# Kernel optimization log

Hardware: AMD Instinct MI355X
Metric: run time of the kernel (lower is better)

## Reference

```python
import jax, jax.numpy as jnp
import numpy as np

T, B, N, M, OUT = 128, 512, 256, 512, 1


def _lin_params(key, out_dim, in_dim, scale=0.05):
    kw, kb = jax.random.split(key)
    W = jax.random.normal(kw, (out_dim, in_dim), dtype=jnp.float32) * scale
    b = jax.random.normal(kb, (out_dim,), dtype=jnp.float32) * scale
    return W, b


def setup_inputs() -> dict:
    key = jax.random.key(0)
    ks = jax.random.split(key, 10)
    x = jax.random.normal(ks[0], (T, B, N), dtype=jnp.float32)
    h0 = jnp.zeros((B, M), dtype=jnp.float32)
    c0 = jnp.zeros((B, M), dtype=jnp.float32)
    # nn.LSTM(n, m): weight_ih (4m,n), weight_hh (4m,m), biases (4m,), gate order i,f,g,o
    Wih, b_ih = _lin_params(ks[1], 4 * M, N)
    Whh, b_hh = _lin_params(ks[2], 4 * M, M)
    We_w, We_b = _lin_params(ks[3], T, 2 * M)   # We: Linear(2m, T)
    Ue_w, Ue_b = _lin_params(ks[4], T, T)       # Ue: Linear(T, T)
    ve_w, ve_b = _lin_params(ks[5], 1, T)       # ve: Linear(T, 1)
    Ud_w, Ud_b = _lin_params(ks[6], M, M)       # Ud: Linear(m, m)
    vd_w, vd_b = _lin_params(ks[7], 1, M)       # vd: Linear(m, 1)
    out_w, out_b = _lin_params(ks[8], OUT, M)   # out: Linear(m, output_dim)
    return dict(x=x, h0=h0, c0=c0, Wih=Wih, Whh=Whh, b_ih=b_ih, b_hh=b_hh,
                We_w=We_w, We_b=We_b, Ue_w=Ue_w, Ue_b=Ue_b, ve_w=ve_w, ve_b=ve_b,
                Ud_w=Ud_w, Ud_b=Ud_b, vd_w=vd_w, vd_b=vd_b, out_w=out_w, out_b=out_b)


def reference(x, h0, c0, Wih, Whh, b_ih, b_hh, We_w, We_b, Ue_w, Ue_b,
              ve_w, ve_b, Ud_w, Ud_b, vd_w, vd_b, out_w, out_b):
    # x: (T, B, n) time-major; dropout_p=0 (eval) -> identity.
    x_perm = jnp.transpose(x, (1, 2, 0))                      # (B, n, T)
    # Ue(x) is independent of the recurrent state; compute once (same math).
    Ue_x = jnp.einsum('bnt,st->bns', x_perm, Ue_w) + Ue_b     # (B, n, T)

    def step(carry, xt):
        h, c = carry                                          # (B, m) each
        hc = jnp.concatenate([h, c], axis=-1)                 # (B, 2m)
        we = hc @ We_w.T + We_b                               # (B, T)
        e = jnp.tanh(we[:, None, :] + Ue_x) @ ve_w[0] + ve_b[0]   # (B, n)
        alpha = jax.nn.softmax(e, axis=1)                     # softmax over n
        x_tilde = alpha * xt                                  # (B, n)
        # LSTM cell (PyTorch gate order i, f, g, o)
        gates = x_tilde @ Wih.T + b_ih + h @ Whh.T + b_hh     # (B, 4m)
        i, f, g, o = jnp.split(gates, 4, axis=-1)
        c_new = jax.nn.sigmoid(f) * c + jax.nn.sigmoid(i) * jnp.tanh(g)
        h_new = jax.nn.sigmoid(o) * jnp.tanh(c_new)
        return (h_new, c_new), h_new

    (_, _), h_seq = jax.lax.scan(step, (h0, c0), x)           # h_seq: (T, B, m)

    # temporal attention over encoder hidden states
    h = jnp.transpose(h_seq, (1, 0, 2))                       # (B, T, m)
    l = jnp.tanh(h @ Ud_w.T + Ud_b) @ vd_w[0] + vd_b[0]       # (B, T)
    beta = jax.nn.softmax(l, axis=1)                          # (B, T)
    ctx = jnp.einsum('bt,btm->bm', beta, h)                   # (B, m)
    logits = ctx @ out_w.T + out_b                            # (B, output_dim)
    return logits, beta
```

## Files before the change

kernel.cpp:

```cpp
#include <hip/hip_runtime.h>
#include <math.h>

#define T_ 128
#define B_ 512
#define N_ 256
#define M_ 512
#define G_ 2048
#define NBLK 256
#define GSZ 32
#define KC_ 24

typedef unsigned long long ull;
typedef __attribute__((ext_vector_type(8))) short short8v;
typedef __attribute__((ext_vector_type(4))) float float4v;

__device__ __forceinline__ float ld_dev(const float* p) {
    return __hip_atomic_load(const_cast<float*>(p), __ATOMIC_RELAXED,
                             __HIP_MEMORY_SCOPE_AGENT);
}
__device__ __forceinline__ void st_dev(float* p, float v) {
    __hip_atomic_store(p, v, __ATOMIC_RELAXED, __HIP_MEMORY_SCOPE_AGENT);
}
__device__ __forceinline__ ull ld_dev64(const ull* p) {
    return __hip_atomic_load(const_cast<ull*>(p), __ATOMIC_RELAXED,
                             __HIP_MEMORY_SCOPE_AGENT);
}
__device__ __forceinline__ void st_dev64(ull* p, ull v) {
    __hip_atomic_store(p, v, __ATOMIC_RELAXED, __HIP_MEMORY_SCOPE_AGENT);
}

__device__ __forceinline__ float fast_tanh(float x) {
    float e = __expf(2.f * x);
    return 1.f - __fdividef(2.f, e + 1.f);
}
__device__ __forceinline__ float fast_sig(float x) {
    return __fdividef(1.f, 1.f + __expf(-x));
}

__device__ __forceinline__ unsigned short bf16_rne(float f) {
    unsigned u = __float_as_uint(f);
    return (unsigned short)((u + 0x7FFFu + ((u >> 16) & 1u)) >> 16);
}
__device__ __forceinline__ float bf16_tof(unsigned short h) {
    return __uint_as_float(((unsigned)h) << 16);
}
__device__ __forceinline__ ull pack4(const unsigned short* s) {
    return (ull)s[0] | ((ull)s[1] << 16) | ((ull)s[2] << 32) | ((ull)s[3] << 48);
}

__device__ __forceinline__ void group_bar(int* gbar, int goal) {
    __syncthreads();
    if (threadIdx.x == 0) {
        asm volatile("s_waitcnt vmcnt(0)" ::: "memory");
        __hip_atomic_fetch_add(gbar, 1, __ATOMIC_RELAXED,
                               __HIP_MEMORY_SCOPE_AGENT);
        while (__hip_atomic_load(gbar, __ATOMIC_RELAXED,
                                 __HIP_MEMORY_SCOPE_AGENT) < goal) {
            __builtin_amdgcn_s_sleep(1);
        }
    }
    __syncthreads();
}

__global__ __launch_bounds__(256) void prep_bg(
    const float* __restrict__ bih, const float* __restrict__ bhh,
    float* __restrict__ bg)
{
    int rp = blockIdx.x * 256 + threadIdx.x;
    if (rp < 2048) {
        int m = rp >> 2, g = rp & 3;
        int row = g * 512 + m;
        bg[rp] = bih[row] + bhh[row];
    }
}

__global__ __launch_bounds__(256) void prep_wt(
    const float* __restrict__ Wih, const float* __restrict__ Whh,
    uint4* __restrict__ Wt_hi, uint4* __restrict__ Wt_lo)
{
    int uid = blockIdx.x * 256 + threadIdx.x;
    int ct = uid / (KC_ * 64);
    int rem = uid % (KC_ * 64);
    int kc = rem >> 6, lane = rem & 63;
    int col = ct * 16 + (lane & 15);
    int m = col >> 2, gi = col & 3;
    int grow = gi * 512 + m;
    int quad = lane >> 4;
    union { unsigned short s[8]; uint4 v; } hi, lo;
#pragma unroll
    for (int j = 0; j < 8; j++) {
        int k = kc * 32 + quad * 8 + j;
        float v = (k < 256) ? Wih[(size_t)grow * 256 + k]
                            : Whh[(size_t)grow * 512 + (k - 256)];
        hi.s[j] = bf16_rne(v);
        lo.s[j] = bf16_rne(v - bf16_tof(hi.s[j]));
    }
    Wt_hi[uid] = hi.v;
    Wt_lo[uid] = lo.v;
}

__global__ __launch_bounds__(256) void prep_wep(
    const float* __restrict__ We_w, float* __restrict__ We_p)
{
    int idx = blockIdx.x * 256 + threadIdx.x;
    int q = idx >> 9, rest = idx & 511, s = rest >> 2, j = rest & 3;
    We_p[idx] = We_w[s * 1024 + q * 4 + j];
}

__global__ __launch_bounds__(256) void ue_pre(
    const float* __restrict__ x, const float* __restrict__ Ue_w,
    const float* __restrict__ Ue_b, unsigned* __restrict__ ue_pk)
{
    const int b = blockIdx.y;
    const int s0 = blockIdx.x * 32;
    const int n = threadIdx.x;
    __shared__ float xs[32][256];
    __shared__ float uws[32][32];

    float acc[32];
#pragma unroll
    for (int i = 0; i < 32; i++) acc[i] = 0.f;

#pragma unroll 1
    for (int tc = 0; tc < 4; tc++) {
        __syncthreads();
#pragma unroll
        for (int tt = 0; tt < 32; tt++)
            xs[tt][n] = x[(size_t)(tc * 32 + tt) * (B_ * N_) + b * N_ + n];
#pragma unroll
        for (int q = 0; q < 4; q++) {
            int e = q * 256 + n;
            int s = e >> 5, tt = e & 31;
            uws[s][tt] = Ue_w[(s0 + s) * T_ + tc * 32 + tt];
        }
        __syncthreads();
        float xr[32];
#pragma unroll
        for (int tt = 0; tt < 32; tt++) xr[tt] = xs[tt][n];
#pragma unroll
        for (int s = 0; s < 32; s++) {
            float a = acc[s];
#pragma unroll
            for (int tt = 0; tt < 32; tt++) a += xr[tt] * uws[s][tt];
            acc[s] = a;
        }
    }
#pragma unroll
    for (int i = 0; i < 16; i++) {
        float v0 = (acc[2 * i] + Ue_b[s0 + 2 * i]) * 2.0f;
        float v1 = (acc[2 * i + 1] + Ue_b[s0 + 2 * i + 1]) * 2.0f;
        unsigned pk = (unsigned)bf16_rne(v0) | ((unsigned)bf16_rne(v1) << 16);
        ue_pk[((size_t)b * 64 + (s0 >> 1) + i) * 256 + n] = pk;
    }
}

__global__ __launch_bounds__(512, 1) void scan_persist(
    const float* __restrict__ x, const float* __restrict__ h0,
    const float* __restrict__ We_p, const float* __restrict__ We_b,
    const float* __restrict__ ve_w, const unsigned* __restrict__ ue_pk,
    const short8v* __restrict__ Wt_hi, const short8v* __restrict__ Wt_lo,
    const float* __restrict__ bg,
    float* __restrict__ cbuf, float* __restrict__ hseq,
    ull* __restrict__ At_hi, ull* __restrict__ At_lo, int* bar)
{
    const int tid = threadIdx.x;
    const int blk = blockIdx.x;
    const int g = blk >> 5;
    const int sg = blk & 31;
    int* gbar = bar + g * 32;

    __shared__ __align__(16) float hcA[1024];
    __shared__ __align__(16) float hcB[1024];
    __shared__ float wepartA[512];
    __shared__ float wepartB[512];
    __shared__ __align__(16) float wv[2][256];
    __shared__ float red[16];
    __shared__ float xs[2][256];
    __shared__ float gates_s[64][65];

    const int bA = g * 64 + sg * 2;
    const int bB = bA + 1;
    const int s_ = tid & 127;
    const int qr = tid >> 7;
    const int half = tid >> 8;
    const int tt = tid & 255;
    const int lane = tid & 63;
    const int w = tid >> 6;
    const int rtC = g * 4 + (w & 3);
    const int ctA = sg * 4 + (w >> 2) * 2;
    const int ctB = ctA + 1;
    const int quad = lane >> 4;
    const int mi_c = tid & 15;
    const int b_l0 = tid >> 4;
    const int cidx0 = (g * 64 + b_l0) * M_ + sg * 16 + mi_c;
    const int cidx1 = cidx0 + 32 * M_;

    if (tid < 128) {
        float v = 2.0f * ve_w[tid];
        wv[0][tid * 2 + 1] = v;
        wv[1][tid * 2 + 1] = v;
    }

    const float bgi = bg[sg * 64 + mi_c * 4 + 0];
    const float bgf = bg[sg * 64 + mi_c * 4 + 1];
    const float bgc = bg[sg * 64 + mi_c * 4 + 2];
    const float bgo = bg[sg * 64 + mi_c * 4 + 3];

    unsigned ureg[64];
    {
        const unsigned* up = ue_pk + ((size_t)(bA + half) * 64) * 256 + tt;
#pragma unroll
        for (int i = 0; i < 64; i++) ureg[i] = up[(size_t)i * 256];
    }

#pragma unroll 1
    for (int t = 0; t < T_; t++) {
        const float* hprev = t ? (hseq + (size_t)(t - 1) * (B_ * M_)) : h0;

        {
            hcA[tid]       = ld_dev(hprev + bA * M_ + tid);
            hcA[512 + tid] = ld_dev(cbuf + bA * M_ + tid);
            hcB[tid]       = ld_dev(hprev + bB * M_ + tid);
            hcB[512 + tid] = ld_dev(cbuf + bB * M_ + tid);
            float xv = x[(size_t)t * (B_ * N_) + (bA + half) * N_ + tt];
            __syncthreads();

            if (tid < 128) {
                int rowsel = tid >> 6;
                int q2 = tid & 63;
                int kc = 8 + (q2 >> 2), qd = q2 & 3;
                const float* hcX = rowsel ? hcB : hcA;
                int mb = (kc - 8) * 32 + qd * 8;
                float v[8];
#pragma unroll
                for (int j = 0; j < 8; j++) v[j] = hcX[mb + j];
                int b2 = bA + rowsel;
                int rt = b2 >> 4;
                int ln = qd * 16 + (b2 & 15);
                size_t uidx = ((size_t)(rt * KC_ + kc) * 64 + ln) * 2;
                unsigned short hi[8], lo[8];
#pragma unroll
                for (int j = 0; j < 8; j++) {
                    hi[j] = bf16_rne(v[j]);
                    lo[j] = bf16_rne(v[j] - bf16_tof(hi[j]));
                }
                st_dev64(At_hi + uidx,     pack4(hi));
                st_dev64(At_hi + uidx + 1, pack4(hi + 4));
                st_dev64(At_lo + uidx,     pack4(lo));
                st_dev64(At_lo + uidx + 1, pack4(lo + 4));
            }

            float accA = 0.f, accB = 0.f;
            const float4* wp4 = (const float4*)We_p;
#pragma unroll 4
            for (int q = qr * 64; q < qr * 64 + 64; q++) {
                float4 wq = wp4[q * 128 + s_];
                float4 a = *(const float4*)&hcA[q * 4];
                float4 b2 = *(const float4*)&hcB[q * 4];
                accA += wq.x * a.x + wq.y * a.y + wq.z * a.z + wq.w * a.w;
                accB += wq.x * b2.x + wq.y * b2.y + wq.z * b2.z + wq.w * b2.w;
            }
            wepartA[qr * 128 + s_] = accA;
            wepartB[qr * 128 + s_] = accB;
            __syncthreads();
            if (tid < 128) {
                float wb = We_b[tid];
                wv[0][tid * 2] = (wepartA[tid] + wepartA[128 + tid]
                                + wepartA[256 + tid] + wepartA[384 + tid] + wb) * 2.0f;
                wv[1][tid * 2] = (wepartB[tid] + wepartB[128 + tid]
                                + wepartB[256 + tid] + wepartB[384 + tid] + wb) * 2.0f;
            }
            __syncthreads();

            float e = 0.f;
#pragma unroll
            for (int i = 0; i < 64; i++) {
                unsigned u = ureg[i];
                float4 q = *(const float4*)&wv[half][i * 4];
                float z0 = q.x + __uint_as_float(u << 16);
                float z1 = q.z + __uint_as_float(u & 0xFFFF0000u);
                float r0 = __builtin_amdgcn_rcpf(__expf(z0) + 1.f);
                float r1 = __builtin_amdgcn_rcpf(__expf(z1) + 1.f);
                e = fmaf(-q.y, r0, e);
                e = fmaf(-q.w, r1, e);
            }

            float m = e;
#pragma unroll
            for (int off = 32; off >= 1; off >>= 1)
                m = fmaxf(m, __shfl_xor(m, off));
            if (lane == 0) red[w] = m;
            __syncthreads();
            float mx = fmaxf(fmaxf(red[half * 4 + 0], red[half * 4 + 1]),
                             fmaxf(red[half * 4 + 2], red[half * 4 + 3]));
            float ex = __expf(e - mx);
            float sm = ex;
#pragma unroll
            for (int off = 32; off >= 1; off >>= 1)
                sm += __shfl_xor(sm, off);
            if (lane == 0) red[8 + w] = sm;
            __syncthreads();
            float denom = red[8 + half * 4 + 0] + red[8 + half * 4 + 1]
                        + red[8 + half * 4 + 2] + red[8 + half * 4 + 3];
            float alpha = __fdividef(ex, denom);
            xs[half][tt] = alpha * xv;
            __syncthreads();

            if (tid >= 128 && tid < 192) {
                int u2 = tid - 128;
                int rowsel = u2 >> 5;
                int q2 = u2 & 31;
                int kc = q2 >> 2, qd = q2 & 3;
                int nb = kc * 32 + qd * 8;
                float v[8];
#pragma unroll
                for (int j = 0; j < 8; j++) v[j] = xs[rowsel][nb + j];
                int b2 = bA + rowsel;
                int rt = b2 >> 4;
                int ln = qd * 16 + (b2 & 15);
                size_t uidx = ((size_t)(rt * KC_ + kc) * 64 + ln) * 2;
                unsigned short hi[8], lo[8];
#pragma unroll
                for (int j = 0; j < 8; j++) {
                    hi[j] = bf16_rne(v[j]);
                    lo[j] = bf16_rne(v[j] - bf16_tof(hi[j]));
                }
                st_dev64(At_hi + uidx,     pack4(hi));
                st_dev64(At_hi + uidx + 1, pack4(hi + 4));
                st_dev64(At_lo + uidx,     pack4(lo));
                st_dev64(At_lo + uidx + 1, pack4(lo + 4));
            }
        }
        group_bar(gbar, (t * 2 + 1) * GSZ);

        {
            float cold0 = ld_dev(&cbuf[cidx0]);
            float cold1 = ld_dev(&cbuf[cidx1]);

            float4v acc0 = {0.f, 0.f, 0.f, 0.f};
            float4v acc1 = {0.f, 0.f, 0.f, 0.f};

            size_t aidx = ((size_t)(rtC * KC_ + 0) * 64 + lane) * 2;
            ull pah0 = ld_dev64(At_hi + aidx), pah1 = ld_dev64(At_hi + aidx + 1);
            ull pal0 = ld_dev64(At_lo + aidx), pal1 = ld_dev64(At_lo + aidx + 1);
            short8v pw0h = Wt_hi[(ctA * KC_ + 0) * 64 + lane];
            short8v pw0l = Wt_lo[(ctA * KC_ + 0) * 64 + lane];
            short8v pw1h = Wt_hi[(ctB * KC_ + 0) * 64 + lane];
            short8v pw1l = Wt_lo[(ctB * KC_ + 0) * 64 + lane];

#pragma unroll 1
            for (int kc = 0; kc < KC_; kc++) {
                ull ah0 = pah0, ah1 = pah1, al0 = pal0, al1 = pal1;
                short8v w0h = pw0h, w0l = pw0l, w1h = pw1h, w1l = pw1l;
                if (kc + 1 < KC_) {
                    size_t ai = ((size_t)(rtC * KC_ + kc + 1) * 64 + lane) * 2;
                    pah0 = ld_dev64(At_hi + ai); pah1 = ld_dev64(At_hi + ai + 1);
                    pal0 = ld_dev64(At_lo + ai); pal1 = ld_dev64(At_lo + ai + 1);
                    pw0h = Wt_hi[(ctA * KC_ + kc + 1) * 64 + lane];
                    pw0l = Wt_lo[(ctA * KC_ + kc + 1) * 64 + lane];
                    pw1h = Wt_hi[(ctB * KC_ + kc + 1) * 64 + lane];
                    pw1l = Wt_lo[(ctB * KC_ + kc + 1) * 64 + lane];
                }
                union { ull u[2]; short8v s; } aH, aL;
                aH.u[0] = ah0; aH.u[1] = ah1;
                aL.u[0] = al0; aL.u[1] = al1;
                acc0 = __builtin_amdgcn_mfma_f32_16x16x32_bf16(aH.s, w0h, acc0, 0, 0, 0);
                acc1 = __builtin_amdgcn_mfma_f32_16x16x32_bf16(aH.s, w1h, acc1, 0, 0, 0);
                acc0 = __builtin_amdgcn_mfma_f32_16x16x32_bf16(aH.s, w0l, acc0, 0, 0, 0);
                acc1 = __builtin_amdgcn_mfma_f32_16x16x32_bf16(aH.s, w1l, acc1, 0, 0, 0);
                acc0 = __builtin_amdgcn_mfma_f32_16x16x32_bf16(aL.s, w0h, acc0, 0, 0, 0);
                acc1 = __builtin_amdgcn_mfma_f32_16x16x32_bf16(aL.s, w1h, acc1, 0, 0, 0);
            }

            const int r0 = (w & 3) * 16;
            const int c0l = (w >> 2) * 32;
#pragma unroll
            for (int r = 0; r < 4; r++) {
                gates_s[r0 + quad * 4 + r][c0l + (lane & 15)] = acc0[r];
                gates_s[r0 + quad * 4 + r][c0l + 16 + (lane & 15)] = acc1[r];
            }
            __syncthreads();

            float* hseq_t = hseq + (size_t)t * (B_ * M_);
            {
                float gi = gates_s[b_l0][mi_c * 4 + 0] + bgi;
                float gf = gates_s[b_l0][mi_c * 4 + 1] + bgf;
                float gc = gates_s[b_l0][mi_c * 4 + 2] + bgc;
                float go = gates_s[b_l0][mi_c * 4 + 3] + bgo;
                float cn = fast_sig(gf) * cold0 + fast_sig(gi) * fast_tanh(gc);
                st_dev(&cbuf[cidx0], cn);
                st_dev(&hseq_t[cidx0], fast_sig(go) * fast_tanh(cn));
            }
            {
                float gi = gates_s[b_l0 + 32][mi_c * 4 + 0] + bgi;
                float gf = gates_s[b_l0 + 32][mi_c * 4 + 1] + bgf;
                float gc = gates_s[b_l0 + 32][mi_c * 4 + 2] + bgc;
                float go = gates_s[b_l0 + 32][mi_c * 4 + 3] + bgo;
                float cn = fast_sig(gf) * cold1 + fast_sig(gi) * fast_tanh(gc);
                st_dev(&cbuf[cidx1], cn);
                st_dev(&hseq_t[cidx1], fast_sig(go) * fast_tanh(cn));
            }
        }
        group_bar(gbar, (t * 2 + 2) * GSZ);
    }
}

__global__ __launch_bounds__(256) void gemm_l(
    const float* __restrict__ A1,
    const float* __restrict__ W1,
    const float* __restrict__ bias1,
    const float* __restrict__ vw, float* __restrict__ lout)
{
    __shared__ float As[16][68];
    __shared__ float Ws[16][68];
    __shared__ float rsum[64];

    const int tid = threadIdx.x;
    const int tx = tid & 15, ty = tid >> 4;
    const int row0 = blockIdx.y * 64;
    const int col0 = blockIdx.x * 64;
    const int li = tid >> 2;
    const int lk4 = (tid & 3) * 4;

    float acc[4][4];
#pragma unroll
    for (int r = 0; r < 4; r++)
#pragma unroll
        for (int cc = 0; cc < 4; cc++) acc[r][cc] = 0.f;

    float4 av = *(const float4*)&A1[(size_t)(row0 + li) * M_ + lk4];
    float4 wvv = *(const float4*)&W1[(size_t)(col0 + li) * M_ + lk4];
#pragma unroll 1
    for (int kk = 0; kk < 512; kk += 16) {
        __syncthreads();
        As[lk4 + 0][li] = av.x; As[lk4 + 1][li] = av.y;
        As[lk4 + 2][li] = av.z; As[lk4 + 3][li] = av.w;
        Ws[lk4 + 0][li] = wvv.x; Ws[lk4 + 1][li] = wvv.y;
        Ws[lk4 + 2][li] = wvv.z; Ws[lk4 + 3][li] = wvv.w;
        __syncthreads();
        if (kk + 16 < 512) {
            av = *(const float4*)&A1[(size_t)(row0 + li) * M_ + kk + 16 + lk4];
            wvv = *(const float4*)&W1[(size_t)(col0 + li) * M_ + kk + 16 + lk4];
        }
#pragma unroll
        for (int k = 0; k < 16; k++) {
            float4 a = *(const float4*)&As[k][ty * 4];
            float4 w2 = *(const float4*)&Ws[k][tx * 4];
            acc[0][0] += a.x * w2.x; acc[0][1] += a.x * w2.y;
            acc[0][2] += a.x * w2.z; acc[0][3] += a.x * w2.w;
            acc[1][0] += a.y * w2.x; acc[1][1] += a.y * w2.y;
            acc[1][2] += a.y * w2.z; acc[1][3] += a.y * w2.w;
            acc[2][0] += a.z * w2.x; acc[2][1] += a.z * w2.y;
            acc[2][2] += a.z * w2.z; acc[2][3] += a.z * w2.w;
            acc[3][0] += a.w * w2.x; acc[3][1] += a.w * w2.y;
            acc[3][2] += a.w * w2.z; acc[3][3] += a.w * w2.w;
        }
    }

    __syncthreads();
    if (tid < 64) rsum[tid] = 0.f;
    __syncthreads();
    float part[4] = {0.f, 0.f, 0.f, 0.f};
#pragma unroll
    for (int r = 0; r < 4; r++)
#pragma unroll
        for (int cc = 0; cc < 4; cc++) {
            int gc = col0 + tx * 4 + cc;
            part[r] += fast_tanh(acc[r][cc] + bias1[gc]) * vw[gc];
        }
#pragma unroll
    for (int r = 0; r < 4; r++)
        atomicAdd(&rsum[ty * 4 + r], part[r]);
    __syncthreads();
    if (tid < 64) {
        int gr = row0 + tid;
        int b = gr & 511, t = gr >> 9;
        atomicAdd(&lout[b * 128 + t], rsum[tid]);
    }
}

__global__ __launch_bounds__(512) void final_kernel(
    const float* __restrict__ lbuf, const float* __restrict__ hseq,
    const float* __restrict__ out_w, const float* __restrict__ out_b,
    float* __restrict__ out)
{
    const int b = blockIdx.x;
    const int tid = threadIdx.x;
    __shared__ float beta_s[128];
    __shared__ float red[512];

    float lv = (tid < 128) ? lbuf[b * 128 + tid] : -1e30f;
    red[tid] = lv; __syncthreads();
    for (int off = 256; off >= 1; off >>= 1) {
        if (tid < off) red[tid] = fmaxf(red[tid], red[tid + off]);
        __syncthreads();
    }
    float mx = red[0]; __syncthreads();
    float ex = (tid < 128) ? __expf(lv - mx) : 0.f;
    red[tid] = ex; __syncthreads();
    for (int off = 256; off >= 1; off >>= 1) {
        if (tid < off) red[tid] += red[tid + off];
        __syncthreads();
    }
    float denom = red[0];
    if (tid < 128) {
        float bt = ex / denom;
        beta_s[tid] = bt;
        out[512 + b * 128 + tid] = bt;
    }
    __syncthreads();

    float ctx = 0.f;
#pragma unroll 4
    for (int t = 0; t < 128; t++)
        ctx += beta_s[t] * hseq[(size_t)t * (B_ * M_) + b * M_ + tid];

    red[tid] = ctx * out_w[tid]; __syncthreads();
    for (int off = 256; off >= 1; off >>= 1) {
        if (tid < off) red[tid] += red[tid + off];
        __syncthreads();
    }
    if (tid == 0) out[b] = red[0] + out_b[0];
}

extern "C" void kernel_launch(void* const* d_in, const int* in_sizes, int n_in,
                              void* d_out, int out_size, void* d_ws, size_t ws_size,
                              hipStream_t stream)
{
    const float* x    = (const float*)d_in[0];
    const float* h0   = (const float*)d_in[1];
    const float* c0   = (const float*)d_in[2];
    const float* Wih  = (const float*)d_in[3];
    const float* Whh  = (const float*)d_in[4];
    const float* b_ih = (const float*)d_in[5];
    const float* b_hh = (const float*)d_in[6];
    const float* We_w = (const float*)d_in[7];
    const float* We_b = (const float*)d_in[8];
    const float* Ue_w = (const float*)d_in[9];
    const float* Ue_b = (const float*)d_in[10];
    const float* ve_w = (const float*)d_in[11];
    const float* Ud_w = (const float*)d_in[13];
    const float* Ud_b = (const float*)d_in[14];
    const float* vd_w = (const float*)d_in[15];
    const float* out_w = (const float*)d_in[17];
    const float* out_b = (const float*)d_in[18];
    float* out = (float*)d_out;

    float* ws    = (float*)d_ws;
    float* ue_pk = ws;
    float* lbuf  = ws;
    float* hseq  = ue_pk + 8388608;
    float* cbuf  = hseq + 33554432;
    float* We_p  = cbuf + 262144;
    float* bgv   = We_p + 131072;
    float* At_hi = bgv + 2048;
    float* At_lo = At_hi + 196608;
    float* Wt_hi = At_lo + 196608;
    float* Wt_lo = Wt_hi + 786432;
    int*   bar   = (int*)(Wt_lo + 786432);

    hipMemcpyAsync(cbuf, c0, (size_t)B_ * M_ * 4, hipMemcpyDeviceToDevice, stream);
    hipMemsetAsync(bar, 0, 8 * 32 * 4, stream);

    prep_bg<<<8, 256, 0, stream>>>(b_ih, b_hh, bgv);
    prep_wt<<<768, 256, 0, stream>>>(Wih, Whh, (uint4*)Wt_hi, (uint4*)Wt_lo);
    prep_wep<<<512, 256, 0, stream>>>(We_w, We_p);
    ue_pre<<<dim3(4, 512), 256, 0, stream>>>(x, Ue_w, Ue_b, (unsigned*)ue_pk);

    scan_persist<<<NBLK, 512, 0, stream>>>(
        x, h0, We_p, We_b, ve_w, (const unsigned*)ue_pk,
        (const short8v*)Wt_hi, (const short8v*)Wt_lo, bgv,
        cbuf, hseq, (ull*)At_hi, (ull*)At_lo, bar);

    hipMemsetAsync(lbuf, 0, (size_t)B_ * T_ * 4, stream);
    gemm_l<<<dim3(8, 1024), 256, 0, stream>>>(hseq, Ud_w, Ud_b, vd_w, lbuf);
    final_kernel<<<512, 512, 0, stream>>>(lbuf, hseq, out_w, out_b, out);
}
```

Before: 4.520 ms.

## Compute We partials in LSTM tail with MFMA and double-buffer recurrent operands

Moves the per-step We·[h,c] projection out of the attention phase. Each block now computes partial products for its own 16-column slice of h and c with split-bf16 MFMA at the end of the previous step and writes them to a global slab; the next step sums 32 partials. The cell state now stays in registers, the h operand is packed into a double-buffered At array inside the tail, and a grid-wide start barrier is added. This drops the per-step global reload of full h/c rows and the scalar fp32 We loop, at the cost of extra global partial stores and loads plus a bigger shared-memory footprint.

Result: slower. 6.313 ms (+39.7%).

```diff
diff --git a/kernel.cpp b/kernel.cpp
--- a/kernel.cpp
+++ b/kernel.cpp
@@ -99,12 +99,27 @@
     Wt_lo[uid] = lo.v;
 }
 
-__global__ __launch_bounds__(256) void prep_wep(
-    const float* __restrict__ We_w, float* __restrict__ We_p)
-{
-    int idx = blockIdx.x * 256 + threadIdx.x;
-    int q = idx >> 9, rest = idx & 511, s = rest >> 2, j = rest & 3;
-    We_p[idx] = We_w[s * 1024 + q * 4 + j];
+__global__ __launch_bounds__(256) void prep_wes(
+    const float* __restrict__ We_w, uint4* __restrict__ Wes_hi,
+    uint4* __restrict__ Wes_lo)
+{
+    int uid = blockIdx.x * 256 + threadIdx.x;
+    int sg = uid >> 9;
+    int rem = uid & 511;
+    int st = rem >> 6, lane = rem & 63;
+    int s = st * 16 + (lane & 15);
+    int quad = lane >> 4;
+    union { unsigned short s[8]; uint4 v; } hi, lo;
+#pragma unroll
+    for (int j = 0; j < 8; j++) {
+        int kk = quad * 8 + j;
+        int k = (kk < 16) ? (sg * 16 + kk) : (512 + sg * 16 + (kk - 16));
+        float v = We_w[s * 1024 + k];
+        hi.s[j] = bf16_rne(v);
+        lo.s[j] = bf16_rne(v - bf16_tof(hi.s[j]));
+    }
+    Wes_hi[uid] = hi.v;
+    Wes_lo[uid] = lo.v;
 }
 
 __global__ __launch_bounds__(256) void ue_pre(
@@ -156,12 +171,16 @@
 
 __global__ __launch_bounds__(512, 1) void scan_persist(
     const float* __restrict__ x, const float* __restrict__ h0,
-    const float* __restrict__ We_p, const float* __restrict__ We_b,
-    const float* __restrict__ ve_w, const unsigned* __restrict__ ue_pk,
+    const float* __restrict__ c0,
+    const float* __restrict__ We_b, const float* __restrict__ ve_w,
+    const unsigned* __restrict__ ue_pk,
     const short8v* __restrict__ Wt_hi, const short8v* __restrict__ Wt_lo,
+    const short8v* __restrict__ Wes_hi, const short8v* __restrict__ Wes_lo,
     const float* __restrict__ bg,
-    float* __restrict__ cbuf, float* __restrict__ hseq,
-    ull* __restrict__ At_hi, ull* __restrict__ At_lo, int* bar)
+    float* __restrict__ hseq, float* __restrict__ wepart,
+    ull* __restrict__ At_hi0, ull* __restrict__ At_lo0,
+    ull* __restrict__ At_hi1, ull* __restrict__ At_lo1,
+    int* bar, int* gcount)
 {
     const int tid = threadIdx.x;
     const int blk = blockIdx.x;
@@ -169,19 +188,16 @@
     const int sg = blk & 31;
     int* gbar = bar + g * 32;
 
-    __shared__ __align__(16) float hcA[1024];
-    __shared__ __align__(16) float hcB[1024];
-    __shared__ float wepartA[512];
-    __shared__ float wepartB[512];
     __shared__ __align__(16) float wv[2][256];
     __shared__ float red[16];
     __shared__ float xs[2][256];
     __shared__ float gates_s[64][65];
+    __shared__ __align__(16) float hn_s[64][20];
+    __shared__ __align__(16) float cn_s[64][20];
+    __shared__ short8v wes_hi_s[512];
+    __shared__ short8v wes_lo_s[512];
 
     const int bA = g * 64 + sg * 2;
-    const int bB = bA + 1;
-    const int s_ = tid & 127;
-    const int qr = tid >> 7;
     const int half = tid >> 8;
     const int tt = tid & 255;
     const int lane = tid & 63;
@@ -206,69 +222,122 @@
     const float bgc = bg[sg * 64 + mi_c * 4 + 2];
     const float bgo = bg[sg * 64 + mi_c * 4 + 3];
 
+    wes_hi_s[tid] = Wes_hi[sg * 512 + tid];
+    wes_lo_s[tid] = Wes_lo[sg * 512 + tid];
+
+    float cst0 = c0[cidx0];
+    float cst1 = c0[cidx1];
+
     unsigned ureg[64];
     {
         const unsigned* up = ue_pk + ((size_t)(bA + half) * 64) * 256 + tt;
 #pragma unroll
         for (int i = 0; i < 64; i++) ureg[i] = up[(size_t)i * 256];
     }
+    asm volatile("s_waitcnt vmcnt(0)" ::: "memory");
+    __syncthreads();
+    if (tid == 0) {
+        __hip_atomic_fetch_add(gcount, 1, __ATOMIC_RELAXED,
+                               __HIP_MEMORY_SCOPE_AGENT);
+        while (__hip_atomic_load(gcount, __ATOMIC_RELAXED,
+                                 __HIP_MEMORY_SCOPE_AGENT) < NBLK) {
+            __builtin_amdgcn_s_sleep(1);
+        }
+    }
+    __syncthreads();
+
+    auto tail = [&](ull* nAh, ull* nAl) {
+        if (tid < 128) {
+            int rt_l = tid >> 5;
+            int q    = (tid >> 4) & 1;
+            int b_lo = tid & 15;
+            int b_local = rt_l * 16 + b_lo;
+            float v[8];
+#pragma unroll
+            for (int j = 0; j < 8; j++) v[j] = hn_s[b_local][q * 8 + j];
+            int kc = 8 + (sg >> 1);
+            int ln = (2 * (sg & 1) + q) * 16 + b_lo;
+            size_t uidx = ((size_t)((g * 4 + rt_l) * KC_ + kc) * 64 + ln) * 2;
+            unsigned short hi[8], lo[8];
+#pragma unroll
+            for (int j = 0; j < 8; j++) {
+                hi[j] = bf16_rne(v[j]);
+                lo[j] = bf16_rne(v[j] - bf16_tof(hi[j]));
+            }
+            st_dev64(nAh + uidx,     pack4(hi));
+            st_dev64(nAh + uidx + 1, pack4(hi + 4));
+            st_dev64(nAl + uidx,     pack4(lo));
+            st_dev64(nAl + uidx + 1, pack4(lo + 4));
+        }
+        {
+            int bt = w & 3;
+            int sth = (w >> 2) * 4;
+            int bb = bt * 16 + (lane & 15);
+            float a[8];
+#pragma unroll
+            for (int j = 0; j < 8; j++)
+                a[j] = (quad < 2) ? hn_s[bb][(quad & 1) * 8 + j]
+                                  : cn_s[bb][(quad & 1) * 8 + j];
+            union { unsigned short s[8]; short8v v; } ah, al;
+#pragma unroll
+            for (int j = 0; j < 8; j++) {
+                ah.s[j] = bf16_rne(a[j]);
+                al.s[j] = bf16_rne(a[j] - bf16_tof(ah.s[j]));
+            }
+            float* slab = wepart + ((size_t)(g * 32 + sg) * 64) * 128;
+#pragma unroll
+            for (int i = 0; i < 4; i++) {
+                short8v bh = wes_hi_s[(sth + i) * 64 + lane];
+                short8v bl2 = wes_lo_s[(sth + i) * 64 + lane];
+                float4v wp = {0.f, 0.f, 0.f, 0.f};
+                wp = __builtin_amdgcn_mfma_f32_16x16x32_bf16(al.v, bh, wp, 0, 0, 0);
+                wp = __builtin_amdgcn_mfma_f32_16x16x32_bf16(ah.v, bl2, wp, 0, 0, 0);
+                wp = __builtin_amdgcn_mfma_f32_16x16x32_bf16(ah.v, bh, wp, 0, 0, 0);
+                int s = (sth + i) * 16 + (lane & 15);
+                float* dst = slab + (size_t)(bt * 16 + quad * 4) * 128 + s;
+                st_dev(dst + 0 * 128, wp[0]);
+                st_dev(dst + 1 * 128, wp[1]);
+                st_dev(dst + 2 * 128, wp[2]);
+                st_dev(dst + 3 * 128, wp[3]);
+            }
+        }
+    };
+
+    {
+        int mi = tid & 15;
+        int bl = tid >> 4;
+        size_t base = (size_t)(g * 64 + bl) * M_ + sg * 16 + mi;
+        hn_s[bl][mi]      = h0[base];
+        hn_s[bl + 32][mi] = h0[base + (size_t)32 * M_];
+        cn_s[bl][mi]      = c0[base];
+        cn_s[bl + 32][mi] = c0[base + (size_t)32 * M_];
+    }
+    __syncthreads();
+    tail(At_hi0, At_lo0);
+
+    int bgoal = GSZ;
+    group_bar(gbar, bgoal); bgoal += GSZ;
 
 #pragma unroll 1
     for (int t = 0; t < T_; t++) {
-        const float* hprev = t ? (hseq + (size_t)(t - 1) * (B_ * M_)) : h0;
+        const int cur = t & 1;
+        const ull* Ah_c = cur ? At_hi1 : At_hi0;
+        const ull* Al_c = cur ? At_lo1 : At_lo0;
+        ull* nAh = cur ? At_hi0 : At_hi1;
+        ull* nAl = cur ? At_lo0 : At_lo1;
 
         {
-            hcA[tid]       = ld_dev(hprev + bA * M_ + tid);
-            hcA[512 + tid] = ld_dev(cbuf + bA * M_ + tid);
-            hcB[tid]       = ld_dev(hprev + bB * M_ + tid);
-            hcB[512 + tid] = ld_dev(cbuf + bB * M_ + tid);
             float xv = x[(size_t)t * (B_ * N_) + (bA + half) * N_ + tt];
-            __syncthreads();
-
-            if (tid < 128) {
-                int rowsel = tid >> 6;
-                int q2 = tid & 63;
-                int kc = 8 + (q2 >> 2), qd = q2 & 3;
-                const float* hcX = rowsel ? hcB : hcA;
-                int mb = (kc - 8) * 32 + qd * 8;
-                float v[8];
-#pragma unroll
-                for (int j = 0; j < 8; j++) v[j] = hcX[mb + j];
-                int b2 = bA + rowsel;
-                int rt = b2 >> 4;
-                int ln = qd * 16 + (b2 & 15);
-                size_t uidx = ((size_t)(rt * KC_ + kc) * 64 + ln) * 2;
-                unsigned short hi[8], lo[8];
-#pragma unroll
-                for (int j = 0; j < 8; j++) {
-                    hi[j] = bf16_rne(v[j]);
-                    lo[j] = bf16_rne(v[j] - bf16_tof(hi[j]));
-                }
-                st_dev64(At_hi + uidx,     pack4(hi));
-                st_dev64(At_hi + uidx + 1, pack4(hi + 4));
-                st_dev64(At_lo + uidx,     pack4(lo));
-                st_dev64(At_lo + uidx + 1, pack4(lo + 4));
-            }
-
-            float accA = 0.f, accB = 0.f;
-            const float4* wp4 = (const float4*)We_p;
-#pragma unroll 4
-            for (int q = qr * 64; q < qr * 64 + 64; q++) {
-                float4 wq = wp4[q * 128 + s_];
-                float4 a = *(const float4*)&hcA[q * 4];
-                float4 b2 = *(const float4*)&hcB[q * 4];
-                accA += wq.x * a.x + wq.y * a.y + wq.z * a.z + wq.w * a.w;
-                accB += wq.x * b2.x + wq.y * b2.y + wq.z * b2.z + wq.w * b2.w;
-            }
-            wepartA[qr * 128 + s_] = accA;
-            wepartB[qr * 128 + s_] = accB;
-            __syncthreads();
-            if (tid < 128) {
-                float wb = We_b[tid];
-                wv[0][tid * 2] = (wepartA[tid] + wepartA[128 + tid]
-                                + wepartA[256 + tid] + wepartA[384 + tid] + wb) * 2.0f;
-                wv[1][tid * 2] = (wepartB[tid] + wepartB[128 + tid]
-                                + wepartB[256 + tid] + wepartB[384 + tid] + wb) * 2.0f;
+            if (tid < 256) {
+                int half2 = tid >> 7;
+                int s = tid & 127;
+                const float* wp = wepart
+                    + ((size_t)(g * 32) * 64 + (sg * 2 + half2)) * 128 + s;
+                float sum = 0.f;
+#pragma unroll
+                for (int src = 0; src < 32; src++)
+                    sum += ld_dev(wp + (size_t)src * 64 * 128);
+                wv[half2][2 * s] = 2.0f * (sum + We_b[s]);
             }
             __syncthreads();
 
@@ -325,24 +394,21 @@
                     hi[j] = bf16_rne(v[j]);
                     lo[j] = bf16_rne(v[j] - bf16_tof(hi[j]));
                 }
-                st_dev64(At_hi + uidx,     pack4(hi));
-                st_dev64(At_hi + uidx + 1, pack4(hi + 4));
-                st_dev64(At_lo + uidx,     pack4(lo));
-                st_dev64(At_lo + uidx + 1, pack4(lo + 4));
-            }
-        }
-        group_bar(gbar, (t * 2 + 1) * GSZ);
+                st_dev64((ull*)Ah_c + uidx,     pack4(hi));
+                st_dev64((ull*)Ah_c + uidx + 1, pack4(hi + 4));
+                st_dev64((ull*)Al_c + uidx,     pack4(lo));
+                st_dev64((ull*)Al_c + uidx + 1, pack4(lo + 4));
+            }
+        }
+        group_bar(gbar, bgoal); bgoal += GSZ;
 
         {
-            float cold0 = ld_dev(&cbuf[cidx0]);
-            float cold1 = ld_dev(&cbuf[cidx1]);
-
             float4v acc0 = {0.f, 0.f, 0.f, 0.f};
             float4v acc1 = {0.f, 0.f, 0.f, 0.f};
 
             size_t aidx = ((size_t)(rtC * KC_ + 0) * 64 + lane) * 2;
-            ull pah0 = ld_dev64(At_hi + aidx), pah1 = ld_dev64(At_hi + aidx + 1);
-            ull pal0 = ld_dev64(At_lo + aidx), pal1 = ld_dev64(At_lo + aidx + 1);
+            ull pah0 = ld_dev64(Ah_c + aidx), pah1 = ld_dev64(Ah_c + aidx + 1);
+            ull pal0 = ld_dev64(Al_c + aidx), pal1 = ld_dev64(Al_c + aidx + 1);
             short8v pw0h = Wt_hi[(ctA * KC_ + 0) * 64 + lane];
             short8v pw0l = Wt_lo[(ctA * KC_ + 0) * 64 + lane];
             short8v pw1h = Wt_hi[(ctB * KC_ + 0) * 64 + lane];
@@ -354,8 +420,8 @@
                 short8v w0h = pw0h, w0l = pw0l, w1h = pw1h, w1l = pw1l;
                 if (kc + 1 < KC_) {
                     size_t ai = ((size_t)(rtC * KC_ + kc + 1) * 64 + lane) * 2;
-                    pah0 = ld_dev64(At_hi + ai); pah1 = ld_dev64(At_hi + ai + 1);
-                    pal0 = ld_dev64(At_lo + ai); pal1 = ld_dev64(At_lo + ai + 1);
+                    pah0 = ld_dev64(Ah_c + ai); pah1 = ld_dev64(Ah_c + ai + 1);
+                    pal0 = ld_dev64(Al_c + ai); pal1 = ld_dev64(Al_c + ai + 1);
                     pw0h = Wt_hi[(ctA * KC_ + kc + 1) * 64 + lane];
                     pw0l = Wt_lo[(ctA * KC_ + kc + 1) * 64 + lane];
                     pw1h = Wt_hi[(ctB * KC_ + kc + 1) * 64 + lane];
@@ -387,21 +453,29 @@
                 float gf = gates_s[b_l0][mi_c * 4 + 1] + bgf;
                 float gc = gates_s[b_l0][mi_c * 4 + 2] + bgc;
                 float go = gates_s[b_l0][mi_c * 4 + 3] + bgo;
-                float cn = fast_sig(gf) * cold0 + fast_sig(gi) * fast_tanh(gc);
-                st_dev(&cbuf[cidx0], cn);
-                st_dev(&hseq_t[cidx0], fast_sig(go) * fast_tanh(cn));
+                float cn = fast_sig(gf) * cst0 + fast_sig(gi) * fast_tanh(gc);
+                cst0 = cn;
+                float hn = fast_sig(go) * fast_tanh(cn);
+                hseq_t[cidx0] = hn;
+                hn_s[b_l0][mi_c] = hn;
+                cn_s[b_l0][mi_c] = cn;
             }
             {
                 float gi = gates_s[b_l0 + 32][mi_c * 4 + 0] + bgi;
                 float gf = gates_s[b_l0 + 32][mi_c * 4 + 1] + bgf;
                 float gc = gates_s[b_l0 + 32][mi_c * 4 + 2] + bgc;
                 float go = gates_s[b_l0 + 32][mi_c * 4 + 3] + bgo;
-                float cn = fast_sig(gf) * cold1 + fast_sig(gi) * fast_tanh(gc);
-                st_dev(&cbuf[cidx1], cn);
-                st_dev(&hseq_t[cidx1], fast_sig(go) * fast_tanh(cn));
-            }
-        }
-        group_bar(gbar, (t * 2 + 2) * GSZ);
+                float cn = fast_sig(gf) * cst1 + fast_sig(gi) * fast_tanh(gc);
+                cst1 = cn;
+                float hn = fast_sig(go) * fast_tanh(cn);
+                hseq_t[cidx1] = hn;
+                hn_s[b_l0 + 32][mi_c] = hn;
+                cn_s[b_l0 + 32][mi_c] = cn;
+            }
+            __syncthreads();
+            if (t + 1 < T_) tail(nAh, nAl);
+        }
+        group_bar(gbar, bgoal); bgoal += GSZ;
     }
 }
 
@@ -546,31 +620,36 @@
     const float* out_b = (const float*)d_in[18];
     float* out = (float*)d_out;
 
-    float* ws    = (float*)d_ws;
-    float* ue_pk = ws;
-    float* lbuf  = ws;
-    float* hseq  = ue_pk + 8388608;
-    float* cbuf  = hseq + 33554432;
-    float* We_p  = cbuf + 262144;
-    float* bgv   = We_p + 131072;
-    float* At_hi = bgv + 2048;
-    float* At_lo = At_hi + 196608;
-    float* Wt_hi = At_lo + 196608;
-    float* Wt_lo = Wt_hi + 786432;
-    int*   bar   = (int*)(Wt_lo + 786432);
-
-    hipMemcpyAsync(cbuf, c0, (size_t)B_ * M_ * 4, hipMemcpyDeviceToDevice, stream);
-    hipMemsetAsync(bar, 0, 8 * 32 * 4, stream);
+    float* ws     = (float*)d_ws;
+    float* ue_pk  = ws;
+    float* lbuf   = ws;
+    float* wepart = ws + 4194304;
+    float* hseq   = ws + 8388608;
+    float* At_hi0 = hseq + 33554432;
+    float* At_lo0 = At_hi0 + 196608;
+    float* At_hi1 = At_lo0 + 196608;
+    float* At_lo1 = At_hi1 + 196608;
+    float* Wes_hi = At_lo1 + 196608;
+    float* Wes_lo = Wes_hi + 65536;
+    float* bgv    = Wes_lo + 65536;
+    float* Wt_hi  = bgv + 2048;
+    float* Wt_lo  = Wt_hi + 786432;
+    int*   bar    = (int*)(Wt_lo + 786432);
+
+    hipMemsetAsync(bar, 0, (8 * 32 + 1) * 4, stream);
 
     prep_bg<<<8, 256, 0, stream>>>(b_ih, b_hh, bgv);
     prep_wt<<<768, 256, 0, stream>>>(Wih, Whh, (uint4*)Wt_hi, (uint4*)Wt_lo);
-    prep_wep<<<512, 256, 0, stream>>>(We_w, We_p);
+    prep_wes<<<64, 256, 0, stream>>>(We_w, (uint4*)Wes_hi, (uint4*)Wes_lo);
     ue_pre<<<dim3(4, 512), 256, 0, stream>>>(x, Ue_w, Ue_b, (unsigned*)ue_pk);
 
     scan_persist<<<NBLK, 512, 0, stream>>>(
-        x, h0, We_p, We_b, ve_w, (const unsigned*)ue_pk,
-        (const short8v*)Wt_hi, (const short8v*)Wt_lo, bgv,
-        cbuf, hseq, (ull*)At_hi, (ull*)At_lo, bar);
+        x, h0, c0, We_b, ve_w, (const unsigned*)ue_pk,
+        (const short8v*)Wt_hi, (const short8v*)Wt_lo,
+        (const short8v*)Wes_hi, (const short8v*)Wes_lo, bgv,
+        hseq, wepart,
+        (ull*)At_hi0, (ull*)At_lo0, (ull*)At_hi1, (ull*)At_lo1,
+        bar, bar + 256);
 
     hipMemsetAsync(lbuf, 0, (size_t)B_ * T_ * 4, stream);
     gemm_l<<<dim3(8, 1024), 256, 0, stream>>>(hseq, Ud_w, Ud_b, vd_w, lbuf);
```

## Overlap recurrent h@Whh MFMA with attention phase using double-buffered packed h

Applied to the files above, without the earlier changes.

Splits the LSTM gate GEMM into an x-part and an h-part. The h@Whh MFMA accumulation (16 k-chunks) now runs inside the We projection loop in phase 1, overlapping it with the attention work, and only the 8 x_tilde chunks remain after the group barrier. Each block packs its new h slice into bf16 hi/lo operand buffers at the end of the step, using ping-pong buffers so the next step can read them without an extra barrier. This shortens the critical path between the two barriers, at the cost of more register pressure and an extra shared buffer plus an initial barrier.

After: 6.327 ms. 1.4x slower.

```diff
diff --git a/kernel.cpp b/kernel.cpp
--- a/kernel.cpp
+++ b/kernel.cpp
@@ -161,7 +161,10 @@
     const short8v* __restrict__ Wt_hi, const short8v* __restrict__ Wt_lo,
     const float* __restrict__ bg,
     float* __restrict__ cbuf, float* __restrict__ hseq,
-    ull* __restrict__ At_hi, ull* __restrict__ At_lo, int* bar)
+    ull* __restrict__ Atx_hi, ull* __restrict__ Atx_lo,
+    ull* __restrict__ Ath_hi0, ull* __restrict__ Ath_lo0,
+    ull* __restrict__ Ath_hi1, ull* __restrict__ Ath_lo1,
+    int* bar)
 {
     const int tid = threadIdx.x;
     const int blk = blockIdx.x;
@@ -177,6 +180,7 @@
     __shared__ float red[16];
     __shared__ float xs[2][256];
     __shared__ float gates_s[64][65];
+    __shared__ float hn_s[64][17];
 
     const int bA = g * 64 + sg * 2;
     const int bB = bA + 1;
@@ -213,52 +217,97 @@
         for (int i = 0; i < 64; i++) ureg[i] = up[(size_t)i * 256];
     }
 
+    if (tid < 128) {
+        int rt_l = tid >> 5;
+        int q = (tid >> 4) & 1;
+        int b_lo = tid & 15;
+        int b_local = rt_l * 16 + b_lo;
+        float v[8];
+#pragma unroll
+        for (int j = 0; j < 8; j++)
+            v[j] = h0[(size_t)(g * 64 + b_local) * M_ + sg * 16 + q * 8 + j];
+        unsigned short hi[8], lo[8];
+#pragma unroll
+        for (int j = 0; j < 8; j++) {
+            hi[j] = bf16_rne(v[j]);
+            lo[j] = bf16_rne(v[j] - bf16_tof(hi[j]));
+        }
+        int kh = sg >> 1;
+        int ln = (2 * (sg & 1) + q) * 16 + b_lo;
+        size_t uidx = ((size_t)((g * 4 + rt_l) * 16 + kh) * 64 + ln) * 2;
+        st_dev64(Ath_hi0 + uidx,     pack4(hi));
+        st_dev64(Ath_hi0 + uidx + 1, pack4(hi + 4));
+        st_dev64(Ath_lo0 + uidx,     pack4(lo));
+        st_dev64(Ath_lo0 + uidx + 1, pack4(lo + 4));
+    }
+    int bgoal = GSZ;
+    group_bar(gbar, bgoal); bgoal += GSZ;
+
 #pragma unroll 1
     for (int t = 0; t < T_; t++) {
         const float* hprev = t ? (hseq + (size_t)(t - 1) * (B_ * M_)) : h0;
+        const int par = t & 1;
+        const ull* Hh = par ? Ath_hi1 : Ath_hi0;
+        const ull* Hl = par ? Ath_lo1 : Ath_lo0;
+        ull* nHh = par ? Ath_hi0 : Ath_hi1;
+        ull* nHl = par ? Ath_lo0 : Ath_lo1;
+
+        float4v acc0 = {0.f, 0.f, 0.f, 0.f};
+        float4v acc1 = {0.f, 0.f, 0.f, 0.f};
+        float cold0, cold1;
 
         {
             hcA[tid]       = ld_dev(hprev + bA * M_ + tid);
             hcA[512 + tid] = ld_dev(cbuf + bA * M_ + tid);
             hcB[tid]       = ld_dev(hprev + bB * M_ + tid);
             hcB[512 + tid] = ld_dev(cbuf + bB * M_ + tid);
+            cold0 = ld_dev(&cbuf[cidx0]);
+            cold1 = ld_dev(&cbuf[cidx1]);
             float xv = x[(size_t)t * (B_ * N_) + (bA + half) * N_ + tt];
             __syncthreads();
-
-            if (tid < 128) {
-                int rowsel = tid >> 6;
-                int q2 = tid & 63;
-                int kc = 8 + (q2 >> 2), qd = q2 & 3;
-                const float* hcX = rowsel ? hcB : hcA;
-                int mb = (kc - 8) * 32 + qd * 8;
-                float v[8];
-#pragma unroll
-                for (int j = 0; j < 8; j++) v[j] = hcX[mb + j];
-                int b2 = bA + rowsel;
-                int rt = b2 >> 4;
-                int ln = qd * 16 + (b2 & 15);
-                size_t uidx = ((size_t)(rt * KC_ + kc) * 64 + ln) * 2;
-                unsigned short hi[8], lo[8];
-#pragma unroll
-                for (int j = 0; j < 8; j++) {
-                    hi[j] = bf16_rne(v[j]);
-                    lo[j] = bf16_rne(v[j] - bf16_tof(hi[j]));
-                }
-                st_dev64(At_hi + uidx,     pack4(hi));
-                st_dev64(At_hi + uidx + 1, pack4(hi + 4));
-                st_dev64(At_lo + uidx,     pack4(lo));
-                st_dev64(At_lo + uidx + 1, pack4(lo + 4));
-            }
 
             float accA = 0.f, accB = 0.f;
             const float4* wp4 = (const float4*)We_p;
-#pragma unroll 4
-            for (int q = qr * 64; q < qr * 64 + 64; q++) {
-                float4 wq = wp4[q * 128 + s_];
-                float4 a = *(const float4*)&hcA[q * 4];
-                float4 b2 = *(const float4*)&hcB[q * 4];
-                accA += wq.x * a.x + wq.y * a.y + wq.z * a.z + wq.w * a.w;
-                accB += wq.x * b2.x + wq.y * b2.y + wq.z * b2.z + wq.w * b2.w;
+            const size_t hb = (size_t)rtC * 16 * 64;
+            size_t ai0 = (hb + lane) * 2;
+            ull pah0 = ld_dev64(Hh + ai0), pah1 = ld_dev64(Hh + ai0 + 1);
+            ull pal0 = ld_dev64(Hl + ai0), pal1 = ld_dev64(Hl + ai0 + 1);
+            short8v pw0h = Wt_hi[(ctA * KC_ + 8) * 64 + lane];
+            short8v pw0l = Wt_lo[(ctA * KC_ + 8) * 64 + lane];
+            short8v pw1h = Wt_hi[(ctB * KC_ + 8) * 64 + lane];
+            short8v pw1l = Wt_lo[(ctB * KC_ + 8) * 64 + lane];
+
+#pragma unroll 1
+            for (int i = 0; i < 16; i++) {
+#pragma unroll
+                for (int jq = 0; jq < 4; jq++) {
+                    int q = qr * 64 + i * 4 + jq;
+                    float4 wq = wp4[q * 128 + s_];
+                    float4 a = *(const float4*)&hcA[q * 4];
+                    float4 b2 = *(const float4*)&hcB[q * 4];
+                    accA += wq.x * a.x + wq.y * a.y + wq.z * a.z + wq.w * a.w;
+                    accB += wq.x * b2.x + wq.y * b2.y + wq.z * b2.z + wq.w * b2.w;
+                }
+                ull ah0 = pah0, ah1 = pah1, al0 = pal0, al1 = pal1;
+                short8v w0h = pw0h, w0l = pw0l, w1h = pw1h, w1l = pw1l;
+                if (i + 1 < 16) {
+                    size_t an = (hb + (size_t)(i + 1) * 64 + lane) * 2;
+                    pah0 = ld_dev64(Hh + an); pah1 = ld_dev64(Hh + an + 1);
+                    pal0 = ld_dev64(Hl + an); pal1 = ld_dev64(Hl + an + 1);
+                    pw0h = Wt_hi[(ctA * KC_ + 9 + i) * 64 + lane];
+                    pw0l = Wt_lo[(ctA * KC_ + 9 + i) * 64 + lane];
+                    pw1h = Wt_hi[(ctB * KC_ + 9 + i) * 64 + lane];
+                    pw1l = Wt_lo[(ctB * KC_ + 9 + i) * 64 + lane];
+                }
+                union { ull u[2]; short8v s; } aH, aL;
+                aH.u[0] = ah0; aH.u[1] = ah1;
+                aL.u[0] = al0; aL.u[1] = al1;
+                acc0 = __builtin_amdgcn_mfma_f32_16x16x32_bf16(aH.s, w0h, acc0, 0, 0, 0);
+                acc1 = __builtin_amdgcn_mfma_f32_16x16x32_bf16(aH.s, w1h, acc1, 0, 0, 0);
+                acc0 = __builtin_amdgcn_mfma_f32_16x16x32_bf16(aH.s, w0l, acc0, 0, 0, 0);
+                acc1 = __builtin_amdgcn_mfma_f32_16x16x32_bf16(aH.s, w1l, acc1, 0, 0, 0);
+                acc0 = __builtin_amdgcn_mfma_f32_16x16x32_bf16(aL.s, w0h, acc0, 0, 0, 0);
+                acc1 = __builtin_amdgcn_mfma_f32_16x16x32_bf16(aL.s, w1h, acc1, 0, 0, 0);
             }
             wepartA[qr * 128 + s_] = accA;
             wepartB[qr * 128 + s_] = accB;
@@ -318,44 +367,39 @@
                 int b2 = bA + rowsel;
                 int rt = b2 >> 4;
                 int ln = qd * 16 + (b2 & 15);
-                size_t uidx = ((size_t)(rt * KC_ + kc) * 64 + ln) * 2;
+                size_t uidx = ((size_t)(rt * 8 + kc) * 64 + ln) * 2;
                 unsigned short hi[8], lo[8];
 #pragma unroll
                 for (int j = 0; j < 8; j++) {
                     hi[j] = bf16_rne(v[j]);
                     lo[j] = bf16_rne(v[j] - bf16_tof(hi[j]));
                 }
-                st_dev64(At_hi + uidx,     pack4(hi));
-                st_dev64(At_hi + uidx + 1, pack4(hi + 4));
-                st_dev64(At_lo + uidx,     pack4(lo));
-                st_dev64(At_lo + uidx + 1, pack4(lo + 4));
-            }
-        }
-        group_bar(gbar, (t * 2 + 1) * GSZ);
+                st_dev64(Atx_hi + uidx,     pack4(hi));
+                st_dev64(Atx_hi + uidx + 1, pack4(hi + 4));
+                st_dev64(Atx_lo + uidx,     pack4(lo));
+                st_dev64(Atx_lo + uidx + 1, pack4(lo + 4));
+            }
+        }
+        group_bar(gbar, bgoal); bgoal += GSZ;
 
         {
-            float cold0 = ld_dev(&cbuf[cidx0]);
-            float cold1 = ld_dev(&cbuf[cidx1]);
-
-            float4v acc0 = {0.f, 0.f, 0.f, 0.f};
-            float4v acc1 = {0.f, 0.f, 0.f, 0.f};
-
-            size_t aidx = ((size_t)(rtC * KC_ + 0) * 64 + lane) * 2;
-            ull pah0 = ld_dev64(At_hi + aidx), pah1 = ld_dev64(At_hi + aidx + 1);
-            ull pal0 = ld_dev64(At_lo + aidx), pal1 = ld_dev64(At_lo + aidx + 1);
+            const size_t xb = (size_t)rtC * 8 * 64;
+            size_t aidx = (xb + lane) * 2;
+            ull pah0 = ld_dev64(Atx_hi + aidx), pah1 = ld_dev64(Atx_hi + aidx + 1);
+            ull pal0 = ld_dev64(Atx_lo + aidx), pal1 = ld_dev64(Atx_lo + aidx + 1);
             short8v pw0h = Wt_hi[(ctA * KC_ + 0) * 64 + lane];
             short8v pw0l = Wt_lo[(ctA * KC_ + 0) * 64 + lane];
             short8v pw1h = Wt_hi[(ctB * KC_ + 0) * 64 + lane];
             short8v pw1l = Wt_lo[(ctB * KC_ + 0) * 64 + lane];
 
 #pragma unroll 1
-            for (int kc = 0; kc < KC_; kc++) {
+            for (int kc = 0; kc < 8; kc++) {
                 ull ah0 = pah0, ah1 = pah1, al0 = pal0, al1 = pal1;
                 short8v w0h = pw0h, w0l = pw0l, w1h = pw1h, w1l = pw1l;
-                if (kc + 1 < KC_) {
-                    size_t ai = ((size_t)(rtC * KC_ + kc + 1) * 64 + lane) * 2;
-                    pah0 = ld_dev64(At_hi + ai); pah1 = ld_dev64(At_hi + ai + 1);
-                    pal0 = ld_dev64(At_lo + ai); pal1 = ld_dev64(At_lo + ai + 1);
+                if (kc + 1 < 8) {
+                    size_t ai = (xb + (size_t)(kc + 1) * 64 + lane) * 2;
+                    pah0 = ld_dev64(Atx_hi + ai); pah1 = ld_dev64(Atx_hi + ai + 1);
+                    pal0 = ld_dev64(Atx_lo + ai); pal1 = ld_dev64(Atx_lo + ai + 1);
                     pw0h = Wt_hi[(ctA * KC_ + kc + 1) * 64 + lane];
                     pw0l = Wt_lo[(ctA * KC_ + kc + 1) * 64 + lane];
                     pw1h = Wt_hi[(ctB * KC_ + kc + 1) * 64 + lane];
@@ -388,8 +432,10 @@
                 float gc = gates_s[b_l0][mi_c * 4 + 2] + bgc;
                 float go = gates_s[b_l0][mi_c * 4 + 3] + bgo;
                 float cn = fast_sig(gf) * cold0 + fast_sig(gi) * fast_tanh(gc);
+                float hn = fast_sig(go) * fast_tanh(cn);
                 st_dev(&cbuf[cidx0], cn);
-                st_dev(&hseq_t[cidx0], fast_sig(go) * fast_tanh(cn));
+                st_dev(&hseq_t[cidx0], hn);
+                hn_s[b_l0][mi_c] = hn;
             }
             {
                 float gi = gates_s[b_l0 + 32][mi_c * 4 + 0] + bgi;
@@ -397,11 +443,37 @@
                 float gc = gates_s[b_l0 + 32][mi_c * 4 + 2] + bgc;
                 float go = gates_s[b_l0 + 32][mi_c * 4 + 3] + bgo;
                 float cn = fast_sig(gf) * cold1 + fast_sig(gi) * fast_tanh(gc);
+                float hn = fast_sig(go) * fast_tanh(cn);
                 st_dev(&cbuf[cidx1], cn);
-                st_dev(&hseq_t[cidx1], fast_sig(go) * fast_tanh(cn));
-            }
-        }
-        group_bar(gbar, (t * 2 + 2) * GSZ);
+                st_dev(&hseq_t[cidx1], hn);
+                hn_s[b_l0 + 32][mi_c] = hn;
+            }
+            __syncthreads();
+
+            if (t + 1 < T_ && tid < 128) {
+                int rt_l = tid >> 5;
+                int q = (tid >> 4) & 1;
+                int b_lo = tid & 15;
+                int b_local = rt_l * 16 + b_lo;
+                float v[8];
+#pragma unroll
+                for (int j = 0; j < 8; j++) v[j] = hn_s[b_local][q * 8 + j];
+                unsigned short hi[8], lo[8];
+#pragma unroll
+                for (int j = 0; j < 8; j++) {
+                    hi[j] = bf16_rne(v[j]);
+                    lo[j] = bf16_rne(v[j] - bf16_tof(hi[j]));
+                }
+                int kh = sg >> 1;
+                int ln = (2 * (sg & 1) + q) * 16 + b_lo;
+                size_t uidx = ((size_t)((g * 4 + rt_l) * 16 + kh) * 64 + ln) * 2;
+                st_dev64(nHh + uidx,     pack4(hi));
+                st_dev64(nHh + uidx + 1, pack4(hi + 4));
+                st_dev64(nHl + uidx,     pack4(lo));
+                st_dev64(nHl + uidx + 1, pack4(lo + 4));
+            }
+        }
+        group_bar(gbar, bgoal); bgoal += GSZ;
     }
 }
 
@@ -546,18 +618,22 @@
     const float* out_b = (const float*)d_in[18];
     float* out = (float*)d_out;
 
-    float* ws    = (float*)d_ws;
-    float* ue_pk = ws;
-    float* lbuf  = ws;
-    float* hseq  = ue_pk + 8388608;
-    float* cbuf  = hseq + 33554432;
-    float* We_p  = cbuf + 262144;
-    float* bgv   = We_p + 131072;
-    float* At_hi = bgv + 2048;
-    float* At_lo = At_hi + 196608;
-    float* Wt_hi = At_lo + 196608;
-    float* Wt_lo = Wt_hi + 786432;
-    int*   bar   = (int*)(Wt_lo + 786432);
+    float* ws     = (float*)d_ws;
+    float* ue_pk  = ws;
+    float* lbuf   = ws;
+    float* hseq   = ws + 8388608;
+    float* cbuf   = hseq + 33554432;
+    float* We_p   = cbuf + 262144;
+    float* bgv    = We_p + 131072;
+    float* Atx_hi = bgv + 2048;
+    float* Atx_lo = Atx_hi + 65536;
+    float* Ath_hi0= Atx_lo + 65536;
+    float* Ath_lo0= Ath_hi0 + 131072;
+    float* Ath_hi1= Ath_lo0 + 131072;
+    float* Ath_lo1= Ath_hi1 + 131072;
+    float* Wt_hi  = Ath_lo1 + 131072;
+    float* Wt_lo  = Wt_hi + 786432;
+    int*   bar    = (int*)(Wt_lo + 786432);
 
     hipMemcpyAsync(cbuf, c0, (size_t)B_ * M_ * 4, hipMemcpyDeviceToDevice, stream);
     hipMemsetAsync(bar, 0, 8 * 32 * 4, stream);
@@ -570,7 +646,10 @@
     scan_persist<<<NBLK, 512, 0, stream>>>(
         x, h0, We_p, We_b, ve_w, (const unsigned*)ue_pk,
         (const short8v*)Wt_hi, (const short8v*)Wt_lo, bgv,
-        cbuf, hseq, (ull*)At_hi, (ull*)At_lo, bar);
+        cbuf, hseq,
+        (ull*)Atx_hi, (ull*)Atx_lo,
+        (ull*)Ath_hi0, (ull*)Ath_lo0, (ull*)Ath_hi1, (ull*)Ath_lo1,
+        bar);
 
     hipMemsetAsync(lbuf, 0, (size_t)B_ * T_ * 4, stream);
     gemm_l<<<dim3(8, 1024), 256, 0, stream>>>(hseq, Ud_w, Ud_b, vd_w, lbuf);
```
